# Optimization experiments

Measured on AMD Instinct MI355X. Metric: run time of the kernel, lower is better.

## Reference

```python
import jax, jax.numpy as jnp
import numpy as np

N, E, B, D, H, C = 50000, 800000, 128, 64, 128, 2
EPS = 1e-5


def setup_inputs() -> dict:
    key = jax.random.key(0)
    ks = jax.random.split(key, 12)
    s = 0.1
    return {
        "x": jax.random.normal(ks[0], (N, D), jnp.float32),
        "edge_index": jax.random.randint(ks[1], (2, E), 0, N, jnp.int64),
        "batch": jnp.sort(jax.random.randint(ks[2], (N,), 0, B, jnp.int64)),
        "W_l": jax.random.normal(ks[3], (D, D), jnp.float32) * s,
        "b_l": jnp.zeros((D,), jnp.float32),
        "W_r": jax.random.normal(ks[4], (D, D), jnp.float32) * s,
        "W_res": jax.random.normal(ks[5], (D, D), jnp.float32) * s,
        "b_res": jnp.zeros((D,), jnp.float32),
        "gamma": jnp.ones((D,), jnp.float32),
        "beta": jnp.zeros((D,), jnp.float32),
        "gate_W1": jax.random.normal(ks[6], (D, D), jnp.float32) * s,
        "gate_b1": jnp.zeros((D,), jnp.float32),
        "gate_W2": jax.random.normal(ks[7], (D, 1), jnp.float32) * s,
        "gate_b2": jnp.zeros((1,), jnp.float32),
        "W_p1": jax.random.normal(ks[8], (D, H), jnp.float32) * s,
        "b_p1": jnp.zeros((H,), jnp.float32),
        "W_p2": jax.random.normal(ks[9], (H, C), jnp.float32) * s,
        "b_p2": jnp.zeros((C,), jnp.float32),
    }


def reference(x, edge_index, batch, W_l, b_l, W_r, W_res, b_res, gamma, beta,
              gate_W1, gate_b1, gate_W2, gate_b2, W_p1, b_p1, W_p2, b_p2):
    src, dst = edge_index[0], edge_index[1]
    # SAGEConv, mean aggregation: gather source feats, scatter-mean to target
    agg = jax.ops.segment_sum(x[src], dst, num_segments=N)          # [N, D]
    cnt = jax.ops.segment_sum(jnp.ones((E,), x.dtype), dst, num_segments=N)
    mean = agg / jnp.maximum(cnt, 1.0)[:, None]
    h = mean @ W_l + b_l + x @ W_r                                   # [N, D]
    # dropout is identity (eval mode)
    # BatchNorm1d (training-mode math: biased batch stats)
    mu = jnp.mean(h, axis=0)
    var = jnp.var(h, axis=0)
    h = (h - mu) * jax.lax.rsqrt(var + EPS) * gamma + beta
    # residual projection of the original features
    h = h + x @ W_res + b_res
    # GlobalAttention pooling: per-graph softmax over gate scores
    gate = jax.nn.relu(h @ gate_W1 + gate_b1) @ gate_W2 + gate_b2    # [N, 1]
    g = gate[:, 0]
    gmax = jax.ops.segment_max(g, batch, num_segments=B)
    gmax = jnp.where(jnp.isfinite(gmax), gmax, 0.0)
    e = jnp.exp(g - gmax[batch])
    z = jax.ops.segment_sum(e, batch, num_segments=B)
    alpha = e / jnp.maximum(z, 1e-16)[batch]
    pooled = jax.ops.segment_sum(alpha[:, None] * h, batch, num_segments=B)  # [B, D]
    # 2-layer predictor MLP with ReLU between
    out = jax.nn.relu(pooled @ W_p1 + b_p1) @ W_p2 + b_p2            # [B, C]
    return out
```

## Files before the change

kernel.cpp:

```cpp
#include <hip/hip_runtime.h>
#include <math.h>

#define N_NODES 50000
#define N_EDGES 800000
#define BATCHES 128
#define DIM 64
#define HID 128
#define NCLS 2
#define EPSV 1e-5f
#define MAXD 64

#define EPB1 1024
#define NBLK_SC ((N_EDGES + EPB1 - 1) / EPB1)
#define NBLK 782

#define MREP 4
#define MSTRIDE 32
#define BAR_STRIDE 512

typedef __attribute__((ext_vector_type(8))) short bf16x8;
typedef __attribute__((ext_vector_type(4))) float f32x4;

__device__ __forceinline__ unsigned short f2bf(float f){
  unsigned u = __float_as_uint(f);
  u += 0x7FFFu + ((u >> 16) & 1u);
  return (unsigned short)(u >> 16);
}
__device__ __forceinline__ float bf2f(unsigned short h){
  return __uint_as_float(((unsigned)h) << 16);
}
__device__ __forceinline__ void split2(float f, unsigned short& hi, unsigned short& lo){
  hi = f2bf(f);
  lo = f2bf(f - bf2f(hi));
}
__device__ __forceinline__ uint4 pack8(const unsigned short* s){
  uint4 u;
  u.x = (unsigned)s[0] | ((unsigned)s[1] << 16);
  u.y = (unsigned)s[2] | ((unsigned)s[3] << 16);
  u.z = (unsigned)s[4] | ((unsigned)s[5] << 16);
  u.w = (unsigned)s[6] | ((unsigned)s[7] << 16);
  return u;
}

__device__ __forceinline__ float gload(const float* p){
  return __hip_atomic_load(p, __ATOMIC_RELAXED, __HIP_MEMORY_SCOPE_AGENT);
}

__device__ __forceinline__ void gbar(unsigned* bb, int bx){
  __syncthreads();
  if (threadIdx.x == 0){
    const int k = bx & 7;
    const unsigned quota = (k < (NBLK & 7)) ? (unsigned)(NBLK/8 + 1)
                                            : (unsigned)(NBLK/8);
    unsigned old = __hip_atomic_fetch_add(&bb[k*32], 1u,
                     __ATOMIC_RELAXED, __HIP_MEMORY_SCOPE_AGENT);
    if (old == quota - 1u){
      unsigned r = __hip_atomic_fetch_add(&bb[8*32], 1u,
                     __ATOMIC_RELAXED, __HIP_MEMORY_SCOPE_AGENT);
      if (r == 7u)
        __hip_atomic_store(&bb[9*32], 1u,
                     __ATOMIC_RELAXED, __HIP_MEMORY_SCOPE_AGENT);
    }
    while (__hip_atomic_load(&bb[9*32],
                     __ATOMIC_RELAXED, __HIP_MEMORY_SCOPE_AGENT) == 0u)
      __builtin_amdgcn_s_sleep(32);
  }
  asm volatile("" ::: "memory");
  __syncthreads();
}

__global__ void k_scatter(const int* __restrict__ ei, int* __restrict__ cnt,
                          unsigned short* __restrict__ csr){
  const int e0 = blockIdx.x * EPB1;
  const int e1 = (e0 + EPB1 < N_EDGES) ? e0 + EPB1 : N_EDGES;
  for (int i = e0 + threadIdx.x; i < e1; i += 256){
    int d = ei[N_EDGES + i];
    int s = ei[i];
    int pos = atomicAdd(&cnt[d], 1);
    csr[(size_t)d*MAXD + pos] = (unsigned short)s;
  }
}

__global__ void k_mean(const float* __restrict__ x,
                       const unsigned short* __restrict__ csr,
                       const int* __restrict__ cnt, float* __restrict__ meanb){
  const int node = (blockIdx.x*256 + threadIdx.x) >> 6;
  const int lane = threadIdx.x & 63;
  const int g = lane >> 4, f = lane & 15;
  const int dg = cnt[node];
  const size_t start = (size_t)node * MAXD;
  float4 acc = make_float4(0.f,0.f,0.f,0.f);
  int e = (lane < dg) ? (int)csr[start + lane] : 0;
  int i = 0;
  for (; i + 16 <= dg; i += 16){
    int s0 = __shfl(e, i +      g, 64);
    int s1 = __shfl(e, i + 4  + g, 64);
    int s2 = __shfl(e, i + 8  + g, 64);
    int s3 = __shfl(e, i + 12 + g, 64);
    float4 v0 = *(const float4*)&x[(size_t)s0*DIM + f*4];
    float4 v1 = *(const float4*)&x[(size_t)s1*DIM + f*4];
    float4 v2 = *(const float4*)&x[(size_t)s2*DIM + f*4];
    float4 v3 = *(const float4*)&x[(size_t)s3*DIM + f*4];
    acc.x += v0.x + v1.x + v2.x + v3.x;
    acc.y += v0.y + v1.y + v2.y + v3.y;
    acc.z += v0.z + v1.z + v2.z + v3.z;
    acc.w += v0.w + v1.w + v2.w + v3.w;
  }
  for (; i < dg; i += 4){
    int idx = i + g;
    int srcl = (idx < dg) ? idx : (dg - 1);
    int s = __shfl(e, srcl, 64);
    if (idx < dg){
      float4 v = *(const float4*)&x[(size_t)s*DIM + f*4];
      acc.x += v.x; acc.y += v.y; acc.z += v.z; acc.w += v.w;
    }
  }
  acc.x += __shfl_xor(acc.x, 16, 64); acc.x += __shfl_xor(acc.x, 32, 64);
  acc.y += __shfl_xor(acc.y, 16, 64); acc.y += __shfl_xor(acc.y, 32, 64);
  acc.z += __shfl_xor(acc.z, 16, 64); acc.z += __shfl_xor(acc.z, 32, 64);
  acc.w += __shfl_xor(acc.w, 16, 64); acc.w += __shfl_xor(acc.w, 32, 64);
  if (g == 0){
    float inv = 1.f / fmaxf((float)dg, 1.f);
    float4 r = make_float4(acc.x*inv, acc.y*inv, acc.z*inv, acc.w*inv);
    *(float4*)&meanb[(size_t)node*DIM + f*4] = r;
  }
}

__device__ __forceinline__ void stage_w64(short* sWh, short* sWl_,
                                          const float* __restrict__ W,
                                          int w, int lane){
  const int k0 = 16 * w;
  #pragma unroll
  for (int kc = 0; kc < 2; ++kc){
    unsigned short h[8], l[8];
    #pragma unroll
    for (int i = 0; i < 8; ++i){
      int k = k0 + 8*kc + i;
      split2(W[k*DIM + lane], h[i], l[i]);
    }
    *(uint4*)&sWh[lane*72 + k0 + 8*kc] = pack8(h);
    *(uint4*)&sWl_[lane*72 + k0 + 8*kc] = pack8(l);
  }
}

#define GEMM64(ACC) do { \
  _Pragma("unroll") \
  for (int kt2 = 0; kt2 < 2; ++kt2){ \
    const int ka = kt2*32 + koff; \
    bf16x8 ah = *(const bf16x8*)&sA[0][mrow][ka]; \
    bf16x8 al = *(const bf16x8*)&sA[1][mrow][ka]; \
    _Pragma("unroll") \
    for (int nt = 0; nt < 4; ++nt){ \
      const int nr = nt*16 + jc; \
      bf16x8 bh = *(const bf16x8*)&sB[0][nr][ka]; \
      bf16x8 bo = *(const bf16x8*)&sB[1][nr][ka]; \
      ACC[nt] = __builtin_amdgcn_mfma_f32_16x16x32_bf16(ah, bh, ACC[nt], 0,0,0); \
      ACC[nt] = __builtin_amdgcn_mfma_f32_16x16x32_bf16(al, bh, ACC[nt], 0,0,0); \
      ACC[nt] = __builtin_amdgcn_mfma_f32_16x16x32_bf16(ah, bo, ACC[nt], 0,0,0); \
    } \
  } \
} while(0)

#define STAGE_A(SRC) do { \
  const int row_  = tid >> 2; \
  const int kq_   = (tid & 3) * 16; \
  const int node_ = base + row_; \
  _Pragma("unroll") \
  for (int cc = 0; cc < 4; ++cc){ \
    float4 v = make_float4(0.f,0.f,0.f,0.f); \
    if (node_ < N_NODES) v = *(const float4*)&SRC[(size_t)node_*DIM + kq_ + 4*cc]; \
    unsigned short h_[4], l_[4]; \
    split2(v.x,h_[0],l_[0]); split2(v.y,h_[1],l_[1]); \
    split2(v.z,h_[2],l_[2]); split2(v.w,h_[3],l_[3]); \
    uint2 ph_, pl_; \
    ph_.x = (unsigned)h_[0] | ((unsigned)h_[1]<<16); \
    ph_.y = (unsigned)h_[2] | ((unsigned)h_[3]<<16); \
    pl_.x = (unsigned)l_[0] | ((unsigned)l_[1]<<16); \
    pl_.y = (unsigned)l_[2] | ((unsigned)l_[3]<<16); \
    *(uint2*)&sA[0][row_][kq_ + 4*cc] = ph_; \
    *(uint2*)&sA[1][row_][kq_ + 4*cc] = pl_; \
  } \
} while(0)

__global__ void __launch_bounds__(256, 4) k_mega(
    const float* __restrict__ meanb, const float* __restrict__ x,
    const float* __restrict__ Wl, const float* __restrict__ bl,
    const float* __restrict__ Wr,
    const float* __restrict__ Wres, const float* __restrict__ bres,
    const float* __restrict__ gamma, const float* __restrict__ beta,
    const float* __restrict__ gW1, const float* __restrict__ gb1,
    const float* __restrict__ gW2, const float* __restrict__ gb2,
    const float* __restrict__ Wp1, const float* __restrict__ bp1,
    const float* __restrict__ Wp2, const float* __restrict__ bp2,
    const int* __restrict__ batch,
    float* __restrict__ musum,
    float* __restrict__ zbuf, float* __restrict__ pooled,
    unsigned* __restrict__ bar, float* __restrict__ outp){
  __shared__ __align__(16) short sA[2][64][72];
  __shared__ __align__(16) short sB[2][64][72];
  __shared__ int sb[64];
  __shared__ unsigned long long runmask;
  __shared__ float smu[2*DIM];
  __shared__ float psh[DIM];
  __shared__ float redh[4];

  const int tid  = threadIdx.x;
  const int lane = tid & 63, w = tid >> 6;
  const int jc   = lane & 15;
  const int g16  = w*4 + (lane >> 4);
  const int mrow = 16*w + jc;
  const int koff = (lane >> 4) * 8;
  const int r0   = 16*w + (lane >> 4)*4;
  const int bx   = blockIdx.x;
  const int base = bx * 64;

  float blv[4];
  #pragma unroll
  for (int nt = 0; nt < 4; ++nt) blv[nt] = bl[nt*16 + jc];

  f32x4 acc[4] = {};
  stage_w64(&sB[0][0][0], &sB[1][0][0], Wl, w, lane);
  STAGE_A(meanb);
  __syncthreads();
  GEMM64(acc);
  __syncthreads();
  stage_w64(&sB[0][0][0], &sB[1][0][0], Wr, w, lane);
  STAGE_A(x);
  __syncthreads();
  GEMM64(acc);

  float s1v[4] = {0.f,0.f,0.f,0.f}, s2v[4] = {0.f,0.f,0.f,0.f};
  #pragma unroll
  for (int nt = 0; nt < 4; ++nt){
    #pragma unroll
    for (int r = 0; r < 4; ++r){
      const int node = base + r0 + r;
      float v = acc[nt][r] + blv[nt];
      acc[nt][r] = v;
      if (node < N_NODES){ s1v[nt] += v; s2v[nt] += v*v; }
    }
  }
  __syncthreads();
  {
    float* sred = (float*)&sB[0][0][0];
    #pragma unroll
    for (int nt = 0; nt < 4; ++nt){
      float a = s1v[nt], b = s2v[nt];
      a += __shfl_xor(a, 16, 64); a += __shfl_xor(a, 32, 64);
      b += __shfl_xor(b, 16, 64); b += __shfl_xor(b, 32, 64);
      if ((lane >> 4) == 0){
        sred[0*256 + w*64 + nt*16 + jc] = a;
        sred[1*256 + w*64 + nt*16 + jc] = b;
      }
    }
    __syncthreads();
    const int rep = bx & (MREP-1);
    if (tid < 64){
      float a = sred[tid] + sred[64+tid] + sred[128+tid] + sred[192+tid];
      float b = sred[256+tid] + sred[320+tid] + sred[384+tid] + sred[448+tid];
      atomicAdd(&musum[(size_t)rep*128*MSTRIDE + (size_t)tid*MSTRIDE], a);
      atomicAdd(&musum[(size_t)rep*128*MSTRIDE + (size_t)(64+tid)*MSTRIDE], b);
    }
  }
  gbar(bar, bx);

  if (tid < 64){
    float s1 = 0.f, s2 = 0.f;
    #pragma unroll
    for (int rep = 0; rep < MREP; ++rep){
      s1 += gload(&musum[(size_t)rep*128*MSTRIDE + (size_t)tid*MSTRIDE]);
      s2 += gload(&musum[(size_t)rep*128*MSTRIDE + (size_t)(64+tid)*MSTRIDE]);
    }
    float mu = s1 / (float)N_NODES;
    float var = s2 / (float)N_NODES - mu*mu;
    smu[tid] = mu;
    smu[DIM+tid] = 1.0f / sqrtf(var + EPSV);
  }
  if (tid < 64){
    int nn = base + tid;
    sb[tid] = batch[(nn < N_NODES) ? nn : (N_NODES-1)];
  }
  stage_w64(&sB[0][0][0], &sB[1][0][0], Wres, w, lane);
  __syncthreads();

  float muv[4], invv[4], gav[4], bev[4], brv[4], g1v[4], w2v[4];
  #pragma unroll
  for (int nt = 0; nt < 4; ++nt){
    const int col = nt*16 + jc;
    muv[nt] = smu[col];    invv[nt] = smu[DIM+col];
    gav[nt] = gamma[col];  bev[nt]  = beta[col];
    brv[nt] = bres[col];   g1v[nt]  = gb1[col];
    w2v[nt] = gW2[col];
  }
  const float gb2v = gb2[0];
  if (w == 0){
    bool fl = (lane > 0) && (sb[lane] != sb[lane-1]);
    unsigned long long mm = __ballot(fl);
    if (lane == 0) runmask = mm;
  }

  f32x4 acc2[4] = {};
  GEMM64(acc2);

  #pragma unroll
  for (int nt = 0; nt < 4; ++nt){
    const int col = nt*16 + jc;
    #pragma unroll
    for (int r = 0; r < 4; ++r){
      float v = (acc[nt][r] - muv[nt])*invv[nt]*gav[nt] + bev[nt]
              + brv[nt] + acc2[nt][r];
      acc[nt][r] = v;
      unsigned short hh, ll;
      split2(v, hh, ll);
      sA[0][r0 + r][col] = (short)hh;
      sA[1][r0 + r][col] = (short)ll;
    }
  }
  __syncthreads();
  stage_w64(&sB[0][0][0], &sB[1][0][0], gW1, w, lane);
  __syncthreads();

  f32x4 acc3[4] = {};
  GEMM64(acc3);

  float p[4] = {0.f,0.f,0.f,0.f};
  #pragma unroll
  for (int nt = 0; nt < 4; ++nt){
    #pragma unroll
    for (int r = 0; r < 4; ++r)
      p[r] += fmaxf(acc3[nt][r] + g1v[nt], 0.f) * w2v[nt];
  }
  float ev[4];
  #pragma unroll
  for (int r = 0; r < 4; ++r){
    float t = p[r];
    t += __shfl_xor(t, 1, 64); t += __shfl_xor(t, 2, 64);
    t += __shfl_xor(t, 4, 64); t += __shfl_xor(t, 8, 64);
    const int node = base + r0 + r;
    ev[r] = (node < N_NODES) ? expf(t + gb2v) : 0.f;
  }

  {
    float* sredp = (float*)&sA[0][0][0];
    float* szl   = sredp + 16*64;
    __syncthreads();
    const unsigned long long m = runmask;
    int rstart = 0;
    while (rstart < 64){
      const int bseg = sb[rstart];
      unsigned long long rest = (rstart >= 63) ? 0ull : (m >> (rstart+1));
      const int rend = rest ? (rstart + 1 + __builtin_ctzll(rest)) : 64;
      float pacc[4] = {0.f,0.f,0.f,0.f};
      float zacc = 0.f;
      #pragma unroll
      for (int r = 0; r < 4; ++r){
        const int ln = 4*g16 + r;
        if (ln >= rstart && ln < rend){
          #pragma unroll
          for (int nt = 0; nt < 4; ++nt) pacc[nt] += ev[r]*acc[nt][r];
          zacc += ev[r];
        }
      }
      #pragma unroll
      for (int nt = 0; nt < 4; ++nt) sredp[g16*64 + nt*16 + jc] = pacc[nt];
      if ((lane & 15) == 0) szl[g16] = zacc;
      __syncthreads();
      if (tid < 64){
        float s = 0.f;
        for (int g2 = 0; g2 < 16; ++g2) s += sredp[g2*64 + tid];
        atomicAdd(&pooled[bseg*DIM + tid], s);
      }
      if (tid == 64){
        float sz2 = 0.f;
        for (int g2 = 0; g2 < 16; ++g2) sz2 += szl[g2];
        atomicAdd(&zbuf[bseg], sz2);
      }
      __syncthreads();
      rstart = rend;
    }
  }
  gbar(bar + BAR_STRIDE, bx);

  if (bx < BATCHES){
    const int b = bx;
    const int t = tid;
    if (t < DIM){
      float zz = fmaxf(gload(&zbuf[b]), 1e-16f);
      psh[t] = gload(&pooled[b*DIM + t]) / zz;
    }
    __syncthreads();
    if (t < HID){
      float a = bp1[t];
      #pragma unroll
      for (int d2 = 0; d2 < DIM; ++d2) a = fmaf(psh[d2], Wp1[d2*HID + t], a);
      a = fmaxf(a, 0.f);
      float o0 = a * Wp2[t*NCLS+0];
      float o1 = a * Wp2[t*NCLS+1];
      #pragma unroll
      for (int o = 32; o > 0; o >>= 1){
        o0 += __shfl_down(o0, o, 64); o1 += __shfl_down(o1, o, 64);
      }
      int hw = t >> 6;
      if ((t & 63) == 0){ redh[hw*2+0] = o0; redh[hw*2+1] = o1; }
    }
    __syncthreads();
    if (t == 0){
      outp[b*NCLS+0] = redh[0]+redh[2]+bp2[0];
      outp[b*NCLS+1] = redh[1]+redh[3]+bp2[1];
    }
  }
}

extern "C" void kernel_launch(void* const* d_in, const int* in_sizes, int n_in,
                              void* d_out, int out_size, void* d_ws, size_t ws_size,
                              hipStream_t stream){
  const float* x     = (const float*)d_in[0];
  const int*   ei    = (const int*)d_in[1];
  const int*   batch = (const int*)d_in[2];
  const float* Wl    = (const float*)d_in[3];
  const float* bl    = (const float*)d_in[4];
  const float* Wr    = (const float*)d_in[5];
  const float* Wres  = (const float*)d_in[6];
  const float* bres  = (const float*)d_in[7];
  const float* gamma = (const float*)d_in[8];
  const float* beta  = (const float*)d_in[9];
  const float* gW1   = (const float*)d_in[10];
  const float* gb1   = (const float*)d_in[11];
  const float* gW2   = (const float*)d_in[12];
  const float* gb2   = (const float*)d_in[13];
  const float* Wp1   = (const float*)d_in[14];
  const float* bp1   = (const float*)d_in[15];
  const float* Wp2   = (const float*)d_in[16];
  const float* bp2   = (const float*)d_in[17];
  float* outp = (float*)d_out;

  int*      cnt    = (int*)d_ws;
  float*    zbuf   = (float*)(cnt + N_NODES);
  float*    pooled = zbuf + BATCHES;
  unsigned* bar    = (unsigned*)(pooled + (size_t)BATCHES*DIM);
  float*    musum  = (float*)(bar + 2*BAR_STRIDE);
  float*    meanb  = musum + (size_t)MREP*128*MSTRIDE;
  unsigned short* csr = (unsigned short*)(meanb + (size_t)N_NODES*DIM);

  const size_t zcount = (size_t)N_NODES + BATCHES + (size_t)BATCHES*DIM
                      + 2*BAR_STRIDE + (size_t)MREP*128*MSTRIDE;
  hipMemsetAsync(d_ws, 0, zcount*sizeof(int), stream);

  k_scatter<<<NBLK_SC, 256, 0, stream>>>(ei, cnt, csr);
  k_mean   <<<N_NODES/4, 256, 0, stream>>>(x, csr, cnt, meanb);
  k_mega   <<<NBLK, 256, 0, stream>>>(meanb, x, Wl, bl, Wr, Wres, bres,
                                      gamma, beta, gW1, gb1, gW2, gb2,
                                      Wp1, bp1, Wp2, bp2, batch,
                                      musum, zbuf, pooled, bar, outp);
}
```

Before: 209.1 us.

## Fuse edge scatter and mean aggregation into persistent mega kernel

Moves the edge-to-CSR scatter and the per-node neighbour mean into the persistent k_mega kernel, separated by an extra grid barrier. The mean rows go straight into shared memory instead of a global meanb buffer. The CSR is switched to a transposed 32-bit layout (slot-major across nodes) written with atomic stores. This removes two kernel launches and the global round trip of the mean features. In exchange it adds a third grid-wide barrier, puts the scatter atomics inside a kernel capped at 4 blocks/CU, and doubles the CSR storage width.

Result: no change. 207.7 us (-0.7%).

```diff
diff --git a/kernel.cpp b/kernel.cpp
--- a/kernel.cpp
+++ b/kernel.cpp
@@ -10,9 +10,8 @@
 #define EPSV 1e-5f
 #define MAXD 64
 
-#define EPB1 1024
-#define NBLK_SC ((N_EDGES + EPB1 - 1) / EPB1)
 #define NBLK 782
+#define EPB  1024
 
 #define MREP 4
 #define MSTRIDE 32
@@ -44,6 +43,15 @@
 
 __device__ __forceinline__ float gload(const float* p){
   return __hip_atomic_load(p, __ATOMIC_RELAXED, __HIP_MEMORY_SCOPE_AGENT);
+}
+__device__ __forceinline__ int iload(const int* p){
+  return __hip_atomic_load(p, __ATOMIC_RELAXED, __HIP_MEMORY_SCOPE_AGENT);
+}
+__device__ __forceinline__ unsigned uload(const unsigned* p){
+  return __hip_atomic_load(p, __ATOMIC_RELAXED, __HIP_MEMORY_SCOPE_AGENT);
+}
+__device__ __forceinline__ void ustore(unsigned* p, unsigned v){
+  __hip_atomic_store(p, v, __ATOMIC_RELAXED, __HIP_MEMORY_SCOPE_AGENT);
 }
 
 __device__ __forceinline__ void gbar(unsigned* bb, int bx){
@@ -67,63 +75,6 @@
   }
   asm volatile("" ::: "memory");
   __syncthreads();
-}
-
-__global__ void k_scatter(const int* __restrict__ ei, int* __restrict__ cnt,
-                          unsigned short* __restrict__ csr){
-  const int e0 = blockIdx.x * EPB1;
-  const int e1 = (e0 + EPB1 < N_EDGES) ? e0 + EPB1 : N_EDGES;
-  for (int i = e0 + threadIdx.x; i < e1; i += 256){
-    int d = ei[N_EDGES + i];
-    int s = ei[i];
-    int pos = atomicAdd(&cnt[d], 1);
-    csr[(size_t)d*MAXD + pos] = (unsigned short)s;
-  }
-}
-
-__global__ void k_mean(const float* __restrict__ x,
-                       const unsigned short* __restrict__ csr,
-                       const int* __restrict__ cnt, float* __restrict__ meanb){
-  const int node = (blockIdx.x*256 + threadIdx.x) >> 6;
-  const int lane = threadIdx.x & 63;
-  const int g = lane >> 4, f = lane & 15;
-  const int dg = cnt[node];
-  const size_t start = (size_t)node * MAXD;
-  float4 acc = make_float4(0.f,0.f,0.f,0.f);
-  int e = (lane < dg) ? (int)csr[start + lane] : 0;
-  int i = 0;
-  for (; i + 16 <= dg; i += 16){
-    int s0 = __shfl(e, i +      g, 64);
-    int s1 = __shfl(e, i + 4  + g, 64);
-    int s2 = __shfl(e, i + 8  + g, 64);
-    int s3 = __shfl(e, i + 12 + g, 64);
-    float4 v0 = *(const float4*)&x[(size_t)s0*DIM + f*4];
-    float4 v1 = *(const float4*)&x[(size_t)s1*DIM + f*4];
-    float4 v2 = *(const float4*)&x[(size_t)s2*DIM + f*4];
-    float4 v3 = *(const float4*)&x[(size_t)s3*DIM + f*4];
-    acc.x += v0.x + v1.x + v2.x + v3.x;
-    acc.y += v0.y + v1.y + v2.y + v3.y;
-    acc.z += v0.z + v1.z + v2.z + v3.z;
-    acc.w += v0.w + v1.w + v2.w + v3.w;
-  }
-  for (; i < dg; i += 4){
-    int idx = i + g;
-    int srcl = (idx < dg) ? idx : (dg - 1);
-    int s = __shfl(e, srcl, 64);
-    if (idx < dg){
-      float4 v = *(const float4*)&x[(size_t)s*DIM + f*4];
-      acc.x += v.x; acc.y += v.y; acc.z += v.z; acc.w += v.w;
-    }
-  }
-  acc.x += __shfl_xor(acc.x, 16, 64); acc.x += __shfl_xor(acc.x, 32, 64);
-  acc.y += __shfl_xor(acc.y, 16, 64); acc.y += __shfl_xor(acc.y, 32, 64);
-  acc.z += __shfl_xor(acc.z, 16, 64); acc.z += __shfl_xor(acc.z, 32, 64);
-  acc.w += __shfl_xor(acc.w, 16, 64); acc.w += __shfl_xor(acc.w, 32, 64);
-  if (g == 0){
-    float inv = 1.f / fmaxf((float)dg, 1.f);
-    float4 r = make_float4(acc.x*inv, acc.y*inv, acc.z*inv, acc.w*inv);
-    *(float4*)&meanb[(size_t)node*DIM + f*4] = r;
-  }
 }
 
 __device__ __forceinline__ void stage_w64(short* sWh, short* sWl_,
@@ -183,7 +134,7 @@
 } while(0)
 
 __global__ void __launch_bounds__(256, 4) k_mega(
-    const float* __restrict__ meanb, const float* __restrict__ x,
+    const int* __restrict__ ei, const float* __restrict__ x,
     const float* __restrict__ Wl, const float* __restrict__ bl,
     const float* __restrict__ Wr,
     const float* __restrict__ Wres, const float* __restrict__ bres,
@@ -193,6 +144,7 @@
     const float* __restrict__ Wp1, const float* __restrict__ bp1,
     const float* __restrict__ Wp2, const float* __restrict__ bp2,
     const int* __restrict__ batch,
+    int* __restrict__ cnt, unsigned* __restrict__ csr32,
     float* __restrict__ musum,
     float* __restrict__ zbuf, float* __restrict__ pooled,
     unsigned* __restrict__ bar, float* __restrict__ outp){
@@ -214,13 +166,97 @@
   const int bx   = blockIdx.x;
   const int base = bx * 64;
 
+  {
+    const int e0 = bx * EPB + tid;
+    #pragma unroll
+    for (int q = 0; q < 4; ++q){
+      const int i = e0 + q*256;
+      if (i < N_EDGES){
+        int d = ei[N_EDGES + i];
+        int s = ei[i];
+        int pos = atomicAdd(&cnt[d], 1);
+        ustore(&csr32[(size_t)pos*N_NODES + d], (unsigned)s);
+      }
+    }
+  }
+  gbar(bar, bx);
+
+  {
+    float* sBf = (float*)&sB[0][0][0];
+    const int g = lane >> 4, f = lane & 15;
+    for (int n16 = 0; n16 < 16; ++n16){
+      const int row = w*16 + n16;
+      const int node = base + row;
+      const int dg = (node < N_NODES) ? iload(&cnt[node]) : 0;
+      float4 a4 = make_float4(0.f,0.f,0.f,0.f);
+      int e = 0;
+      if (lane < dg) e = (int)uload(&csr32[(size_t)lane*N_NODES + node]);
+      int i = 0;
+      for (; i + 16 <= dg; i += 16){
+        int s0 = __shfl(e, i +      g, 64);
+        int s1 = __shfl(e, i + 4  + g, 64);
+        int s2 = __shfl(e, i + 8  + g, 64);
+        int s3 = __shfl(e, i + 12 + g, 64);
+        float4 v0 = *(const float4*)&x[(size_t)s0*DIM + f*4];
+        float4 v1 = *(const float4*)&x[(size_t)s1*DIM + f*4];
+        float4 v2 = *(const float4*)&x[(size_t)s2*DIM + f*4];
+        float4 v3 = *(const float4*)&x[(size_t)s3*DIM + f*4];
+        a4.x += v0.x + v1.x + v2.x + v3.x;
+        a4.y += v0.y + v1.y + v2.y + v3.y;
+        a4.z += v0.z + v1.z + v2.z + v3.z;
+        a4.w += v0.w + v1.w + v2.w + v3.w;
+      }
+      for (; i < dg; i += 4){
+        int idx = i + g;
+        int srcl = (idx < dg) ? idx : (dg - 1);
+        int s = __shfl(e, srcl, 64);
+        if (idx < dg){
+          float4 v = *(const float4*)&x[(size_t)s*DIM + f*4];
+          a4.x += v.x; a4.y += v.y; a4.z += v.z; a4.w += v.w;
+        }
+      }
+      a4.x += __shfl_xor(a4.x, 16, 64); a4.x += __shfl_xor(a4.x, 32, 64);
+      a4.y += __shfl_xor(a4.y, 16, 64); a4.y += __shfl_xor(a4.y, 32, 64);
+      a4.z += __shfl_xor(a4.z, 16, 64); a4.z += __shfl_xor(a4.z, 32, 64);
+      a4.w += __shfl_xor(a4.w, 16, 64); a4.w += __shfl_xor(a4.w, 32, 64);
+      if (g == 0){
+        float inv = 1.f / fmaxf((float)dg, 1.f);
+        *(float4*)&sBf[row*64 + 4*f] =
+          make_float4(a4.x*inv, a4.y*inv, a4.z*inv, a4.w*inv);
+      }
+    }
+  }
+  __syncthreads();
+
   float blv[4];
   #pragma unroll
   for (int nt = 0; nt < 4; ++nt) blv[nt] = bl[nt*16 + jc];
 
   f32x4 acc[4] = {};
-  stage_w64(&sB[0][0][0], &sB[1][0][0], Wl, w, lane);
-  STAGE_A(meanb);
+  {
+    float* sBf = (float*)&sB[0][0][0];
+    const int row_ = tid >> 2;
+    const int kq_  = (tid & 3) * 16;
+    float4 mv[4];
+    #pragma unroll
+    for (int cc = 0; cc < 4; ++cc)
+      mv[cc] = *(float4*)&sBf[row_*64 + kq_ + 4*cc];
+    __syncthreads();
+    #pragma unroll
+    for (int cc = 0; cc < 4; ++cc){
+      unsigned short h_[4], l_[4];
+      split2(mv[cc].x,h_[0],l_[0]); split2(mv[cc].y,h_[1],l_[1]);
+      split2(mv[cc].z,h_[2],l_[2]); split2(mv[cc].w,h_[3],l_[3]);
+      uint2 ph_, pl_;
+      ph_.x = (unsigned)h_[0] | ((unsigned)h_[1]<<16);
+      ph_.y = (unsigned)h_[2] | ((unsigned)h_[3]<<16);
+      pl_.x = (unsigned)l_[0] | ((unsigned)l_[1]<<16);
+      pl_.y = (unsigned)l_[2] | ((unsigned)l_[3]<<16);
+      *(uint2*)&sA[0][row_][kq_ + 4*cc] = ph_;
+      *(uint2*)&sA[1][row_][kq_ + 4*cc] = pl_;
+    }
+    stage_w64(&sB[0][0][0], &sB[1][0][0], Wl, w, lane);
+  }
   __syncthreads();
   GEMM64(acc);
   __syncthreads();
@@ -262,7 +298,7 @@
       atomicAdd(&musum[(size_t)rep*128*MSTRIDE + (size_t)(64+tid)*MSTRIDE], b);
     }
   }
-  gbar(bar, bx);
+  gbar(bar + BAR_STRIDE, bx);
 
   if (tid < 64){
     float s1 = 0.f, s2 = 0.f;
@@ -379,7 +415,7 @@
       rstart = rend;
     }
   }
-  gbar(bar + BAR_STRIDE, bx);
+  gbar(bar + 2*BAR_STRIDE, bx);
 
   if (bx < BATCHES){
     const int b = bx;
@@ -438,18 +474,15 @@
   float*    zbuf   = (float*)(cnt + N_NODES);
   float*    pooled = zbuf + BATCHES;
   unsigned* bar    = (unsigned*)(pooled + (size_t)BATCHES*DIM);
-  float*    musum  = (float*)(bar + 2*BAR_STRIDE);
-  float*    meanb  = musum + (size_t)MREP*128*MSTRIDE;
-  unsigned short* csr = (unsigned short*)(meanb + (size_t)N_NODES*DIM);
+  float*    musum  = (float*)(bar + 3*BAR_STRIDE);
+  unsigned* csr32  = (unsigned*)(musum + (size_t)MREP*128*MSTRIDE);
 
   const size_t zcount = (size_t)N_NODES + BATCHES + (size_t)BATCHES*DIM
-                      + 2*BAR_STRIDE + (size_t)MREP*128*MSTRIDE;
+                      + 3*BAR_STRIDE + (size_t)MREP*128*MSTRIDE;
   hipMemsetAsync(d_ws, 0, zcount*sizeof(int), stream);
 
-  k_scatter<<<NBLK_SC, 256, 0, stream>>>(ei, cnt, csr);
-  k_mean   <<<N_NODES/4, 256, 0, stream>>>(x, csr, cnt, meanb);
-  k_mega   <<<NBLK, 256, 0, stream>>>(meanb, x, Wl, bl, Wr, Wres, bres,
-                                      gamma, beta, gW1, gb1, gW2, gb2,
-                                      Wp1, bp1, Wp2, bp2, batch,
-                                      musum, zbuf, pooled, bar, outp);
-}
+  k_mega<<<NBLK, 256, 0, stream>>>(ei, x, Wl, bl, Wr, Wres, bres,
+                                   gamma, beta, gW1, gb1, gW2, gb2,
+                                   Wp1, bp1, Wp2, bp2, batch,
+                                   cnt, csr32, musum, zbuf, pooled, bar, outp);
+}
```
